# Kernel tuning notes

Measured on AMD Instinct MI355X. Metric: run time of the kernel, lower is better.

The kernel has to match this reference:

```python
import jax, jax.numpy as jnp
import numpy as np

N = 50000   # nodes
E = 400000  # edges per relation
R = 3       # relations
IN, HID, C, H = 128, 64, 40, 3  # in_feat, hidden_feat, n_classes, num_heads
NEG_SLOPE = 0.2  # DGL GATConv default leaky_relu slope


def setup_inputs() -> dict:
    key = jax.random.key(0)
    ks = jax.random.split(key, 12)
    feat = jax.random.normal(ks[0], (N, IN), jnp.float32)
    src = jax.random.randint(ks[1], (R, E), 0, N, dtype=jnp.int32)
    dst = jax.random.randint(ks[2], (R, E), 0, N, dtype=jnp.int32)

    def w(k, shape, fan):
        return jax.random.normal(k, shape, jnp.float32) / np.float32(np.sqrt(fan))

    # layer 1: in_feat -> hidden_feat, relu activation
    W1 = w(ks[3], (R, IN, H * HID), IN)
    al1 = w(ks[4], (R, H, HID), HID)
    ar1 = w(ks[5], (R, H, HID), HID)
    b1 = jnp.zeros((R, H * HID), jnp.float32)
    # layer 2: hidden_feat -> n_classes, no activation
    W2 = w(ks[6], (R, HID, H * C), HID)
    al2 = w(ks[7], (R, H, C), C)
    ar2 = w(ks[8], (R, H, C), C)
    b2 = jnp.zeros((R, H * C), jnp.float32)
    return dict(feat=feat, src=src, dst=dst, W1=W1, al1=al1, ar1=ar1, b1=b1,
                W2=W2, al2=al2, ar2=ar2, b2=b2)


def gat_hetero_layer(feat, src, dst, W, al, ar, b, apply_relu):
    """HeteroGraphConv(mean) over R relations, each a GATConv + head-mean."""
    n = feat.shape[0]

    def one_relation(src_r, dst_r, W_r, al_r, ar_r, b_r):
        n_heads, out = al_r.shape
        z = (feat @ W_r).reshape(n, n_heads, out)          # [N,H,out]
        el = jnp.sum(z * al_r, axis=-1)                    # [N,H]
        er = jnp.sum(z * ar_r, axis=-1)                    # [N,H]
        e = jax.nn.leaky_relu(el[src_r] + er[dst_r], NEG_SLOPE)  # [E,H]
        # edge softmax over incoming edges of each dst node
        m = jax.ops.segment_max(e, dst_r, num_segments=n)  # [N,H]
        a = jnp.exp(e - m[dst_r])                          # [E,H]
        s = jax.ops.segment_sum(a, dst_r, num_segments=n)  # [N,H]
        alpha = a / s[dst_r]                               # [E,H]
        msg = alpha[:, :, None] * z[src_r]                 # [E,H,out]
        rst = jax.ops.segment_sum(msg, dst_r, num_segments=n)  # [N,H,out]
        rst = rst + b_r.reshape(n_heads, out)
        if apply_relu:
            rst = jax.nn.relu(rst)
        return rst.mean(axis=1)                            # head mean -> [N,out]

    outs = jax.vmap(one_relation)(src, dst, W, al, ar, b)  # [R,N,out]
    return outs.mean(axis=0)                               # relation mean


def reference(feat, src, dst, W1, al1, ar1, b1, W2, al2, ar2, b2):
    h = gat_hetero_layer(feat, src, dst, W1, al1, ar1, b1, True)
    h = gat_hetero_layer(h, src, dst, W2, al2, ar2, b2, False)
    return h
```

## Files before the change

kernel.cpp:

```cpp
#include <hip/hip_runtime.h>

#define R_   3
#define N_   50000
#define E_   400000
#define IN_  128
#define HID_ 64
#define C_   40
#define H_   3
#define NEG_SLOPE 0.2f
#define LOG2E 1.4426950408889634f

#define SCAN_CHUNK 1024
#define NCH  49
#define NCH2 64

#define MPAD 50048
#define NRT  3128

typedef _Float16 half_t;
typedef _Float16 f16x8 __attribute__((ext_vector_type(8)));
typedef _Float16 f16x4 __attribute__((ext_vector_type(4)));
typedef float float4v __attribute__((ext_vector_type(4)));

template <int V> struct vecT;
template <> struct vecT<4> { typedef f16x4 type; };
template <> struct vecT<8> { typedef f16x8 type; };

__global__ void zero_kernel(float* __restrict__ p, size_t n) {
    size_t i = (size_t)blockIdx.x * blockDim.x + threadIdx.x;
    if (i < n) p[i] = 0.f;
}

__global__ void cast_tiled_kernel(const float* __restrict__ feat, half_t* __restrict__ At) {
    int idx = blockIdx.x * 256 + threadIdx.x;
    const int TOT = NRT * 4 * 64;
    if (idx >= TOT) return;
    int lane = idx & 63;
    int kb = (idx >> 6) & 3;
    int rowtile = idx >> 8;
    int row = rowtile * 16 + (lane & 15);
    int k = kb * 32 + (lane >> 4) * 8;
    f16x8 h = {};
    if (row < N_) {
        const float* p = feat + (size_t)row * IN_ + k;
        float4 a = ((const float4*)p)[0];
        float4 b = ((const float4*)p)[1];
        h[0] = (half_t)a.x; h[1] = (half_t)a.y; h[2] = (half_t)a.z; h[3] = (half_t)a.w;
        h[4] = (half_t)b.x; h[5] = (half_t)b.y; h[6] = (half_t)b.z; h[7] = (half_t)b.w;
    }
    ((f16x8*)At)[idx] = h;
}

template <int K, int NY>
__global__ void bprep_kernel(const float* __restrict__ W, half_t* __restrict__ Bf, int Nc) {
    constexpr int KB = K / 32;
    int idx = blockIdx.x * 256 + threadIdx.x;
    const int TOT = R_ * NY * KB * 4 * 64;
    if (idx >= TOT) return;
    int lane = idx & 63;
    int ct = (idx >> 6) & 3;
    int t = idx >> 8;
    int kb = t % KB; t /= KB;
    int y = t % NY;  int r = t / NY;
    int col = y * 64 + ct * 16 + (lane & 15);
    int k0 = kb * 32 + (lane >> 4) * 8;
    f16x8 h = {};
    if (col < Nc) {
        #pragma unroll
        for (int j = 0; j < 8; ++j)
            h[j] = (half_t)W[((size_t)r * K + k0 + j) * Nc + col];
    }
    ((f16x8*)Bf)[idx] = h;
}

__global__ void hist_kernel(const int* __restrict__ dst, int* __restrict__ deg) {
    int idx = blockIdx.x * 256 + threadIdx.x;
    if (idx < R_ * E_) {
        int r = idx / E_;
        atomicAdd(&deg[r * N_ + dst[idx]], 1);
    }
}

__global__ void scanA_kernel(const int* __restrict__ deg, int* __restrict__ bsum) {
    int r = blockIdx.y, ch = blockIdx.x, tid = threadIdx.x;
    int base = ch * SCAN_CHUNK + tid * 4;
    int s = 0;
    for (int j = 0; j < 4; ++j) {
        int i = base + j;
        if (i < N_) s += deg[r * N_ + i];
    }
    __shared__ int red[256];
    red[tid] = s; __syncthreads();
    for (int off = 128; off; off >>= 1) {
        if (tid < off) red[tid] += red[tid + off];
        __syncthreads();
    }
    if (tid == 0) bsum[r * NCH2 + ch] = red[0];
}

__global__ void scanB_kernel(int* __restrict__ bsum) {
    int w = threadIdx.x >> 6;
    int l = threadIdx.x & 63;
    if (w < R_) {
        int v = (l < NCH) ? bsum[w * NCH2 + l] : 0;
        int s = v;
        #pragma unroll
        for (int off = 1; off < 64; off <<= 1) {
            int t = __shfl_up(s, off);
            if (l >= off) s += t;
        }
        if (l < NCH) bsum[w * NCH2 + l] = s - v;
    }
}

__global__ void scanC_kernel(const int* __restrict__ deg, const int* __restrict__ bsum,
                             int* __restrict__ rowptr, int* __restrict__ cursor) {
    int r = blockIdx.y, ch = blockIdx.x, tid = threadIdx.x;
    int base = ch * SCAN_CHUNK + tid * 4;
    int v[4]; int s = 0;
    for (int j = 0; j < 4; ++j) {
        int i = base + j;
        v[j] = (i < N_) ? deg[r * N_ + i] : 0;
        s += v[j];
    }
    __shared__ int buf[256];
    buf[tid] = s; __syncthreads();
    for (int off = 1; off < 256; off <<= 1) {
        int t2 = (tid >= off) ? buf[tid - off] : 0;
        __syncthreads();
        buf[tid] += t2;
        __syncthreads();
    }
    int excl = buf[tid] - s + bsum[r * NCH2 + ch];
    int run = excl;
    for (int j = 0; j < 4; ++j) {
        int i = base + j;
        if (i < N_) {
            rowptr[r * (N_ + 1) + i] = run;
            cursor[r * N_ + i] = run;
            run += v[j];
        }
    }
    if (ch == 0 && tid == 0) rowptr[r * (N_ + 1) + N_] = E_;
}

__global__ void fill_kernel(const int* __restrict__ src, const int* __restrict__ dst,
                            int* __restrict__ cursor, int* __restrict__ csr_src) {
    int idx = blockIdx.x * 256 + threadIdx.x;
    if (idx < R_ * E_) {
        int r = idx / E_;
        int pos = atomicAdd(&cursor[r * N_ + dst[idx]], 1);
        csr_src[(size_t)r * E_ + pos] = src[idx] * 3;
    }
}

template <int K, int NY, bool FUSE>
__global__ __launch_bounds__(256) void mfma_gemm3_kernel(
        const half_t* __restrict__ At, const half_t* __restrict__ Bf,
        half_t* __restrict__ Z, int Nc,
        const float* __restrict__ al, const float* __restrict__ ar,
        float* __restrict__ el, float* __restrict__ er) {
    constexpr int KB = K / 32;
    int r = blockIdx.z, y = blockIdx.y;
    int wave = threadIdx.x >> 6, lane = threadIdx.x & 63;
    int rowtile = blockIdx.x * 4 + wave;
    const f16x8* Ap = (const f16x8*)At + (size_t)rowtile * KB * 64 + lane;
    const f16x8* Bp = (const f16x8*)Bf + (size_t)(r * NY + y) * KB * 4 * 64 + lane;
    float4v acc[4] = {};
    #pragma unroll
    for (int kb = 0; kb < KB; ++kb) {
        f16x8 af = Ap[kb * 64];
        #pragma unroll
        for (int ct = 0; ct < 4; ++ct) {
            f16x8 bf = Bp[(kb * 4 + ct) * 64];
            acc[ct] = __builtin_amdgcn_mfma_f32_16x16x32_f16(af, bf, acc[ct], 0, 0, 0);
        }
    }
    int lrow = lane & 15, lq = lane >> 4;
    half_t* Zr = Z + (size_t)r * N_ * Nc;
    int rbase = rowtile * 16 + lq * 4;
    int col0 = y * 64;
    float elv[4] = {}, erv[4] = {};
    const float* alp;
    const float* arp;
    if constexpr (FUSE) {
        alp = al + ((size_t)r * H_ + y) * 64;
        arp = ar + ((size_t)r * H_ + y) * 64;
    }
    #pragma unroll
    for (int ct = 0; ct < 4; ++ct) {
        int col = col0 + ct * 16 + lrow;
        if (col >= Nc) continue;
        float wa = 0.f, wb = 0.f;
        if constexpr (FUSE) { wa = alp[ct * 16 + lrow]; wb = arp[ct * 16 + lrow]; }
        #pragma unroll
        for (int g = 0; g < 4; ++g) {
            int row = rbase + g;
            half_t zh = (half_t)acc[ct][g];
            if (row < N_) Zr[(size_t)row * Nc + col] = zh;
            if constexpr (FUSE) {
                float zf = (float)zh;
                elv[g] = fmaf(zf, wa, elv[g]);
                erv[g] = fmaf(zf, wb, erv[g]);
            }
        }
    }
    if constexpr (FUSE) {
        #pragma unroll
        for (int g = 0; g < 4; ++g) {
            #pragma unroll
            for (int m = 1; m < 16; m <<= 1) {
                elv[g] += __shfl_xor(elv[g], m);
                erv[g] += __shfl_xor(erv[g], m);
            }
        }
        if (lrow == 0) {
            #pragma unroll
            for (int g = 0; g < 4; ++g) {
                int row = rbase + g;
                if (row < N_) {
                    size_t o = ((size_t)r * N_ + row) * H_ + y;
                    el[o] = elv[g] * LOG2E;
                    er[o] = erv[g] * LOG2E;
                }
            }
        }
    }
}

template <int Dd>
__global__ __launch_bounds__(256) void attn2_kernel(
        const half_t* __restrict__ z, const float* __restrict__ al,
        const float* __restrict__ ar, float* __restrict__ el,
        float* __restrict__ er) {
    int t = blockIdx.x * 256 + threadIdx.x;
    if (t >= R_ * N_ * H_) return;
    int rn = t / H_, h = t - rn * H_;
    int r = rn / N_;
    const half_t* zrow = z + (size_t)rn * (3 * Dd) + h * Dd;
    const float* alp = al + (r * H_ + h) * Dd;
    const float* arp = ar + (r * H_ + h) * Dd;
    float p0 = 0.f, p1 = 0.f, q0 = 0.f, q1 = 0.f;
    #pragma unroll
    for (int c = 0; c < Dd / 8; ++c) {
        f16x8 zv = *(const f16x8*)(zrow + c * 8);
        #pragma unroll
        for (int j = 0; j < 8; j += 2) {
            float za = (float)zv[j], zb = (float)zv[j + 1];
            p0 += za * alp[c * 8 + j];
            p1 += zb * alp[c * 8 + j + 1];
            q0 += za * arp[c * 8 + j];
            q1 += zb * arp[c * 8 + j + 1];
        }
    }
    el[t] = (p0 + p1) * LOG2E;
    er[t] = (q0 + q1) * LOG2E;
}

template <int Dd, int VEC, bool RELU, typename OutT, bool TILED>
__global__ __launch_bounds__(256) void agg14_kernel(
        const int* __restrict__ rowptr, const int* __restrict__ csr_src,
        const half_t* __restrict__ z, const float* __restrict__ el,
        const float* __restrict__ er, const float* __restrict__ bias,
        OutT* __restrict__ out, float scale) {
    constexpr int ROWH = 3 * Dd;
    constexpr int LPE  = ROWH / VEC;
    constexpr int PH   = Dd / VEC;
    using fv = typename vecT<VEC>::type;
    int n = blockIdx.x * 4 + (threadIdx.x >> 6);
    int lane = threadIdx.x & 63;
    if (n >= N_) return;
    int hf = lane >> 5;
    int sub = lane & 31;
    bool act = sub < LPE;
    int hl = act ? sub / PH : 0;
    int dl = act ? sub - hl * PH : 0;
    int zoff = VEC * sub;
    int ii[R_], ee[R_];
    float ervv[R_];
    #pragma unroll
    for (int r = 0; r < R_; ++r) {
        ii[r] = rowptr[r * (N_ + 1) + n];
        ee[r] = rowptr[r * (N_ + 1) + n + 1];
        ervv[r] = er[((size_t)r * N_ + n) * H_ + hl];
    }
    fv ah[R_] = {};
    float ll[R_] = {};
    while (ii[0] < ee[0] || ii[1] < ee[1] || ii[2] < ee[2]) {
        fv zA[R_], zB[R_];
        float xA[R_], xB[R_];
        bool okA[R_], okB[R_];
        #pragma unroll
        for (int r = 0; r < R_; ++r) {
            const int* cs = csr_src + (size_t)r * E_;
            const half_t* zr = z + (size_t)r * N_ * ROWH;
            const float* elr = el + (size_t)r * N_ * H_;
            int eA = ii[r] + hf, eB = ii[r] + 2 + hf;
            okA[r] = eA < ee[r];
            okB[r] = eB < ee[r];
            int sA = cs[okA[r] ? eA : 0];
            int sB = cs[okB[r] ? eB : 0];
            xA[r] = elr[sA + hl] + ervv[r];
            xB[r] = elr[sB + hl] + ervv[r];
            zA[r] = {}; zB[r] = {};
            if (act) {
                zA[r] = *(const fv*)(zr + (size_t)sA * Dd + zoff);
                zB[r] = *(const fv*)(zr + (size_t)sB * Dd + zoff);
            }
        }
        #pragma unroll
        for (int r = 0; r < R_; ++r) {
            float xa = xA[r]; xa = fmaxf(xa, NEG_SLOPE * xa);
            float xb = xB[r]; xb = fmaxf(xb, NEG_SLOPE * xb);
            float cA = okA[r] ? __builtin_amdgcn_exp2f(xa) : 0.f;
            float cB = okB[r] ? __builtin_amdgcn_exp2f(xb) : 0.f;
            ll[r] += cA + cB;
            half_t hA = (half_t)cA, hB = (half_t)cB;
            fv vA, vB;
            #pragma unroll
            for (int v = 0; v < VEC; ++v) { vA[v] = hA; vB[v] = hB; }
            ah[r] += vA * zA[r] + vB * zB[r];
        }
        #pragma unroll
        for (int r = 0; r < R_; ++r) ii[r] += 4;
    }
    float aa[R_][VEC];
    #pragma unroll
    for (int r = 0; r < R_; ++r)
        #pragma unroll
        for (int v = 0; v < VEC; ++v) aa[r][v] = (float)ah[r][v];
    #pragma unroll
    for (int r = 0; r < R_; ++r) {
        #pragma unroll
        for (int v = 0; v < VEC; ++v) aa[r][v] += __shfl(aa[r][v], lane ^ 32);
        ll[r] += __shfl(ll[r], lane ^ 32);
    }
    float vacc[VEC] = {};
    #pragma unroll
    for (int r = 0; r < R_; ++r) {
        float li = (ll[r] > 0.f) ? 1.f / ll[r] : 0.f;
        const float* br = bias + r * ROWH + hl * Dd + VEC * dl;
        #pragma unroll
        for (int v = 0; v < VEC; ++v) {
            float t = aa[r][v] * li + br[v];
            if (RELU) t = fmaxf(t, 0.f);
            vacc[v] += t;
        }
    }
    int base = lane & 32;
    int p1 = sub + PH;     if (p1 >= LPE) p1 -= LPE;
    int p2 = sub + 2 * PH; if (p2 >= LPE) p2 -= LPE;
    #pragma unroll
    for (int v = 0; v < VEC; ++v)
        vacc[v] += __shfl(vacc[v], base + p1) + __shfl(vacc[v], base + p2);
    int srcl = lane / VEC;
    int cm = lane & (VEC - 1);
    float tv[VEC];
    #pragma unroll
    for (int v = 0; v < VEC; ++v) tv[v] = __shfl(vacc[v], srcl);
    float outv = tv[0];
    #pragma unroll
    for (int v = 1; v < VEC; ++v) outv = (cm == v) ? tv[v] : outv;
    if constexpr (TILED) {
        int rowtile = n >> 4;
        int kb = lane >> 5;
        int fl = (n & 15) + ((lane >> 3) & 3) * 16;
        int elo = lane & 7;
        size_t ho = (((size_t)rowtile * 2 + kb) * 64 + fl) * 8 + elo;
        ((half_t*)out)[ho] = (half_t)(outv * scale);
    } else {
        if (lane < Dd) out[(size_t)n * Dd + lane] = (OutT)(outv * scale);
    }
}

static inline size_t align256(size_t x) { return (x + 255) & ~(size_t)255; }

extern "C" void kernel_launch(void* const* d_in, const int* in_sizes, int n_in,
                              void* d_out, int out_size, void* d_ws, size_t ws_size,
                              hipStream_t stream) {
    const float* feat = (const float*)d_in[0];
    const int*   src  = (const int*)d_in[1];
    const int*   dst  = (const int*)d_in[2];
    const float* W1   = (const float*)d_in[3];
    const float* al1  = (const float*)d_in[4];
    const float* ar1  = (const float*)d_in[5];
    const float* b1   = (const float*)d_in[6];
    const float* W2   = (const float*)d_in[7];
    const float* al2  = (const float*)d_in[8];
    const float* ar2  = (const float*)d_in[9];
    const float* b2   = (const float*)d_in[10];
    float* out = (float*)d_out;

    char* ws = (char*)d_ws;
    size_t off = 0;
    half_t* zbuf  = (half_t*)(ws + off); off += align256((size_t)R_ * N_ * (3 * HID_) * 2);
    half_t* featT = (half_t*)(ws + off); off += align256((size_t)NRT * 4 * 64 * 8 * 2);
    half_t* h1T   = (half_t*)(ws + off); off += align256((size_t)NRT * 2 * 64 * 8 * 2);
    half_t* B1f   = (half_t*)(ws + off); off += align256((size_t)R_ * 3 * 4 * 4 * 64 * 8 * 2);
    half_t* B2f   = (half_t*)(ws + off); off += align256((size_t)R_ * 2 * 2 * 4 * 64 * 8 * 2);
    float* el   = (float*)(ws + off); off += align256((size_t)R_ * N_ * H_ * 4);
    float* er   = (float*)(ws + off); off += align256((size_t)R_ * N_ * H_ * 4);
    int* deg    = (int*)(ws + off);   off += align256((size_t)R_ * N_ * 4);
    int* rowptr = (int*)(ws + off);   off += align256((size_t)R_ * (N_ + 1) * 4);
    int* cursor = (int*)(ws + off);   off += align256((size_t)R_ * N_ * 4);
    int* bsum   = (int*)(ws + off);   off += align256((size_t)R_ * NCH2 * 4);
    int* csr    = (int*)(ws + off);   off += align256((size_t)R_ * E_ * 4);
    (void)ws_size; (void)n_in; (void)in_sizes; (void)out_size;

    const int EDGE_BLOCKS = (R_ * E_ + 255) / 256;
    const int ROW_TILES = (N_ + 63) / 64;
    const int NODE_BLOCKS = (R_ * N_ + 255) / 256;
    const int NODE_WAVES = (N_ + 3) / 4;
    const int ATTN_BLOCKS = (R_ * N_ * H_ + 255) / 256;

    cast_tiled_kernel<<<(NRT * 4 * 64 + 255) / 256, 256, 0, stream>>>(feat, featT);
    bprep_kernel<IN_, 3><<<(R_ * 3 * 4 * 4 * 64 + 255) / 256, 256, 0, stream>>>(W1, B1f, H_ * HID_);
    bprep_kernel<HID_, 2><<<(R_ * 2 * 2 * 4 * 64 + 255) / 256, 256, 0, stream>>>(W2, B2f, H_ * C_);
    zero_kernel<<<7, 256, 0, stream>>>((float*)(h1T + (size_t)3125 * 2 * 512), 1536);

    zero_kernel<<<NODE_BLOCKS, 256, 0, stream>>>((float*)deg, (size_t)R_ * N_);
    hist_kernel<<<EDGE_BLOCKS, 256, 0, stream>>>(dst, deg);
    scanA_kernel<<<dim3(NCH, R_), 256, 0, stream>>>(deg, bsum);
    scanB_kernel<<<1, 192, 0, stream>>>(bsum);
    scanC_kernel<<<dim3(NCH, R_), 256, 0, stream>>>(deg, bsum, rowptr, cursor);
    fill_kernel<<<EDGE_BLOCKS, 256, 0, stream>>>(src, dst, cursor, csr);

    mfma_gemm3_kernel<IN_, 3, true><<<dim3(ROW_TILES, 3, R_), 256, 0, stream>>>(
        featT, B1f, zbuf, H_ * HID_, al1, ar1, el, er);
    agg14_kernel<HID_, 8, true, half_t, true><<<NODE_WAVES, 256, 0, stream>>>(
        rowptr, csr, zbuf, el, er, b1, h1T, 1.f / (H_ * R_));

    mfma_gemm3_kernel<HID_, 2, false><<<dim3(ROW_TILES, 2, R_), 256, 0, stream>>>(
        h1T, B2f, zbuf, H_ * C_, nullptr, nullptr, nullptr, nullptr);
    attn2_kernel<C_><<<ATTN_BLOCKS, 256, 0, stream>>>(zbuf, al2, ar2, el, er);
    agg14_kernel<C_, 4, false, float, false><<<NODE_WAVES, 256, 0, stream>>>(
        rowptr, csr, zbuf, el, er, b2, out, 1.f / (H_ * R_));
}
```

Measured before the change: 449.9 us.

## Merge prep kernels, fold scan pass, batch atomics, software-pipeline aggregation gathers

```diff
diff --git a/kernel.cpp b/kernel.cpp
--- a/kernel.cpp
+++ b/kernel.cpp
@@ -26,35 +26,11 @@
 template <> struct vecT<4> { typedef f16x4 type; };
 template <> struct vecT<8> { typedef f16x8 type; };
 
-__global__ void zero_kernel(float* __restrict__ p, size_t n) {
-    size_t i = (size_t)blockIdx.x * blockDim.x + threadIdx.x;
-    if (i < n) p[i] = 0.f;
-}
-
-__global__ void cast_tiled_kernel(const float* __restrict__ feat, half_t* __restrict__ At) {
-    int idx = blockIdx.x * 256 + threadIdx.x;
-    const int TOT = NRT * 4 * 64;
-    if (idx >= TOT) return;
-    int lane = idx & 63;
-    int kb = (idx >> 6) & 3;
-    int rowtile = idx >> 8;
-    int row = rowtile * 16 + (lane & 15);
-    int k = kb * 32 + (lane >> 4) * 8;
-    f16x8 h = {};
-    if (row < N_) {
-        const float* p = feat + (size_t)row * IN_ + k;
-        float4 a = ((const float4*)p)[0];
-        float4 b = ((const float4*)p)[1];
-        h[0] = (half_t)a.x; h[1] = (half_t)a.y; h[2] = (half_t)a.z; h[3] = (half_t)a.w;
-        h[4] = (half_t)b.x; h[5] = (half_t)b.y; h[6] = (half_t)b.z; h[7] = (half_t)b.w;
-    }
-    ((f16x8*)At)[idx] = h;
-}
 
 template <int K, int NY>
-__global__ void bprep_kernel(const float* __restrict__ W, half_t* __restrict__ Bf, int Nc) {
+__device__ inline void bprep_body(int idx, const float* __restrict__ W,
+                                  half_t* __restrict__ Bf, int Nc) {
     constexpr int KB = K / 32;
-    int idx = blockIdx.x * 256 + threadIdx.x;
     const int TOT = R_ * NY * KB * 4 * 64;
     if (idx >= TOT) return;
     int lane = idx & 63;
@@ -73,9 +49,47 @@
     ((f16x8*)Bf)[idx] = h;
 }
 
+__global__ void prep_kernel(const float* __restrict__ feat, half_t* __restrict__ At,
+                            const float* __restrict__ W1, half_t* __restrict__ B1f,
+                            const float* __restrict__ W2, half_t* __restrict__ B2f,
+                            int* __restrict__ deg, half_t* __restrict__ h1T) {
+    int b = blockIdx.x;
+    if (b < 3128) {
+        int idx = b * 256 + threadIdx.x;
+        int lane = idx & 63;
+        int kb = (idx >> 6) & 3;
+        int rowtile = idx >> 8;
+        int row = rowtile * 16 + (lane & 15);
+        int k = kb * 32 + (lane >> 4) * 8;
+        f16x8 h = {};
+        if (row < N_) {
+            const float* p = feat + (size_t)row * IN_ + k;
+            float4 a = ((const float4*)p)[0];
+            float4 c = ((const float4*)p)[1];
+            h[0] = (half_t)a.x; h[1] = (half_t)a.y; h[2] = (half_t)a.z; h[3] = (half_t)a.w;
+            h[4] = (half_t)c.x; h[5] = (half_t)c.y; h[6] = (half_t)c.z; h[7] = (half_t)c.w;
+        }
+        ((f16x8*)At)[idx] = h;
+    } else if (b < 3164) {
+        bprep_body<IN_, 3>((b - 3128) * 256 + threadIdx.x, W1, B1f, H_ * HID_);
+    } else if (b < 3188) {
+        bprep_body<HID_, 2>((b - 3164) * 256 + threadIdx.x, W2, B2f, H_ * C_);
+    } else if (b < 3774) {
+        int i = (b - 3188) * 256 + threadIdx.x;
+        if (i < R_ * N_) deg[i] = 0;
+    } else {
+        int i = (b - 3774) * 256 + threadIdx.x;
+        if (i < 3072) h1T[(size_t)3125 * 2 * 512 + i] = (half_t)0.f;
+    }
+}
+
 __global__ void hist_kernel(const int* __restrict__ dst, int* __restrict__ deg) {
-    int idx = blockIdx.x * 256 + threadIdx.x;
-    if (idx < R_ * E_) {
+    const int T = (R_ * E_) / 4;
+    int t = blockIdx.x * 256 + threadIdx.x;
+    if (t >= T) return;
+    #pragma unroll
+    for (int j = 0; j < 4; ++j) {
+        int idx = t + j * T;
         int r = idx / E_;
         atomicAdd(&deg[r * N_ + dst[idx]], 1);
     }
@@ -98,24 +112,20 @@
     if (tid == 0) bsum[r * NCH2 + ch] = red[0];
 }
 
-__global__ void scanB_kernel(int* __restrict__ bsum) {
-    int w = threadIdx.x >> 6;
-    int l = threadIdx.x & 63;
-    if (w < R_) {
-        int v = (l < NCH) ? bsum[w * NCH2 + l] : 0;
-        int s = v;
-        #pragma unroll
-        for (int off = 1; off < 64; off <<= 1) {
-            int t = __shfl_up(s, off);
-            if (l >= off) s += t;
-        }
-        if (l < NCH) bsum[w * NCH2 + l] = s - v;
-    }
-}
-
 __global__ void scanC_kernel(const int* __restrict__ deg, const int* __restrict__ bsum,
                              int* __restrict__ rowptr, int* __restrict__ cursor) {
     int r = blockIdx.y, ch = blockIdx.x, tid = threadIdx.x;
+    __shared__ int chbase_s;
+    if (tid < 64) {
+        int v = (tid < NCH) ? bsum[r * NCH2 + tid] : 0;
+        int s = v;
+        #pragma unroll
+        for (int off = 1; off < 64; off <<= 1) {
+            int t = __shfl_up(s, off);
+            if (tid >= off) s += t;
+        }
+        if (tid == ch) chbase_s = s - v;
+    }
     int base = ch * SCAN_CHUNK + tid * 4;
     int v[4]; int s = 0;
     for (int j = 0; j < 4; ++j) {
@@ -131,7 +141,7 @@
         buf[tid] += t2;
         __syncthreads();
     }
-    int excl = buf[tid] - s + bsum[r * NCH2 + ch];
+    int excl = buf[tid] - s + chbase_s;
     int run = excl;
     for (int j = 0; j < 4; ++j) {
         int i = base + j;
@@ -146,12 +156,20 @@
 
 __global__ void fill_kernel(const int* __restrict__ src, const int* __restrict__ dst,
                             int* __restrict__ cursor, int* __restrict__ csr_src) {
-    int idx = blockIdx.x * 256 + threadIdx.x;
-    if (idx < R_ * E_) {
-        int r = idx / E_;
-        int pos = atomicAdd(&cursor[r * N_ + dst[idx]], 1);
-        csr_src[(size_t)r * E_ + pos] = src[idx] * 3;
-    }
+    const int T = (R_ * E_) / 4;
+    int t = blockIdx.x * 256 + threadIdx.x;
+    if (t >= T) return;
+    int pos[4], s3[4], rr[4];
+    #pragma unroll
+    for (int j = 0; j < 4; ++j) {
+        int idx = t + j * T;
+        rr[j] = idx / E_;
+        pos[j] = atomicAdd(&cursor[rr[j] * N_ + dst[idx]], 1);
+        s3[j] = src[idx] * 3;
+    }
+    #pragma unroll
+    for (int j = 0; j < 4; ++j)
+        csr_src[(size_t)rr[j] * E_ + pos[j]] = s3[j];
 }
 
 template <int K, int NY, bool FUSE>
@@ -258,7 +276,7 @@
 }
 
 template <int Dd, int VEC, bool RELU, typename OutT, bool TILED>
-__global__ __launch_bounds__(256) void agg14_kernel(
+__global__ __launch_bounds__(256) void agg15_kernel(
         const int* __restrict__ rowptr, const int* __restrict__ csr_src,
         const half_t* __restrict__ z, const float* __restrict__ el,
         const float* __restrict__ er, const float* __restrict__ bias,
@@ -286,43 +304,86 @@
     }
     fv ah[R_] = {};
     float ll[R_] = {};
-    while (ii[0] < ee[0] || ii[1] < ee[1] || ii[2] < ee[2]) {
-        fv zA[R_], zB[R_];
-        float xA[R_], xB[R_];
-        bool okA[R_], okB[R_];
+    bool any = (ii[0] < ee[0]) | (ii[1] < ee[1]) | (ii[2] < ee[2]);
+    if (any) {
+        int sA_c[R_], sB_c[R_], sA_n[R_], sB_n[R_];
+        fv zA_c[R_], zB_c[R_];
+        float eA_c[R_], eB_c[R_];
         #pragma unroll
         for (int r = 0; r < R_; ++r) {
             const int* cs = csr_src + (size_t)r * E_;
+            int eA = ii[r] + hf, eB = ii[r] + 2 + hf;
+            sA_c[r] = cs[eA < ee[r] ? eA : 0];
+            sB_c[r] = cs[eB < ee[r] ? eB : 0];
+        }
+        #pragma unroll
+        for (int r = 0; r < R_; ++r) {
             const half_t* zr = z + (size_t)r * N_ * ROWH;
             const float* elr = el + (size_t)r * N_ * H_;
-            int eA = ii[r] + hf, eB = ii[r] + 2 + hf;
-            okA[r] = eA < ee[r];
-            okB[r] = eB < ee[r];
-            int sA = cs[okA[r] ? eA : 0];
-            int sB = cs[okB[r] ? eB : 0];
-            xA[r] = elr[sA + hl] + ervv[r];
-            xB[r] = elr[sB + hl] + ervv[r];
-            zA[r] = {}; zB[r] = {};
+            eA_c[r] = elr[sA_c[r] + hl];
+            eB_c[r] = elr[sB_c[r] + hl];
+            zA_c[r] = {}; zB_c[r] = {};
             if (act) {
-                zA[r] = *(const fv*)(zr + (size_t)sA * Dd + zoff);
-                zB[r] = *(const fv*)(zr + (size_t)sB * Dd + zoff);
+                zA_c[r] = *(const fv*)(zr + (size_t)sA_c[r] * Dd + zoff);
+                zB_c[r] = *(const fv*)(zr + (size_t)sB_c[r] * Dd + zoff);
             }
         }
         #pragma unroll
         for (int r = 0; r < R_; ++r) {
-            float xa = xA[r]; xa = fmaxf(xa, NEG_SLOPE * xa);
-            float xb = xB[r]; xb = fmaxf(xb, NEG_SLOPE * xb);
-            float cA = okA[r] ? __builtin_amdgcn_exp2f(xa) : 0.f;
-            float cB = okB[r] ? __builtin_amdgcn_exp2f(xb) : 0.f;
-            ll[r] += cA + cB;
-            half_t hA = (half_t)cA, hB = (half_t)cB;
-            fv vA, vB;
-            #pragma unroll
-            for (int v = 0; v < VEC; ++v) { vA[v] = hA; vB[v] = hB; }
-            ah[r] += vA * zA[r] + vB * zB[r];
-        }
-        #pragma unroll
-        for (int r = 0; r < R_; ++r) ii[r] += 4;
+            const int* cs = csr_src + (size_t)r * E_;
+            int eA = ii[r] + 4 + hf, eB = ii[r] + 6 + hf;
+            sA_n[r] = cs[eA < ee[r] ? eA : 0];
+            sB_n[r] = cs[eB < ee[r] ? eB : 0];
+        }
+        while (true) {
+            fv zA_n[R_], zB_n[R_];
+            float eA_n[R_], eB_n[R_];
+            #pragma unroll
+            for (int r = 0; r < R_; ++r) {
+                const half_t* zr = z + (size_t)r * N_ * ROWH;
+                const float* elr = el + (size_t)r * N_ * H_;
+                eA_n[r] = elr[sA_n[r] + hl];
+                eB_n[r] = elr[sB_n[r] + hl];
+                zA_n[r] = {}; zB_n[r] = {};
+                if (act) {
+                    zA_n[r] = *(const fv*)(zr + (size_t)sA_n[r] * Dd + zoff);
+                    zB_n[r] = *(const fv*)(zr + (size_t)sB_n[r] * Dd + zoff);
+                }
+            }
+            int sA_2[R_], sB_2[R_];
+            #pragma unroll
+            for (int r = 0; r < R_; ++r) {
+                const int* cs = csr_src + (size_t)r * E_;
+                int eA = ii[r] + 8 + hf, eB = ii[r] + 10 + hf;
+                sA_2[r] = cs[eA < ee[r] ? eA : 0];
+                sB_2[r] = cs[eB < ee[r] ? eB : 0];
+            }
+            #pragma unroll
+            for (int r = 0; r < R_; ++r) {
+                int eA = ii[r] + hf, eB = ii[r] + 2 + hf;
+                bool okA = eA < ee[r], okB = eB < ee[r];
+                float xa = eA_c[r] + ervv[r]; xa = fmaxf(xa, NEG_SLOPE * xa);
+                float xb = eB_c[r] + ervv[r]; xb = fmaxf(xb, NEG_SLOPE * xb);
+                float cA = okA ? __builtin_amdgcn_exp2f(xa) : 0.f;
+                float cB = okB ? __builtin_amdgcn_exp2f(xb) : 0.f;
+                ll[r] += cA + cB;
+                half_t hA = (half_t)cA, hB = (half_t)cB;
+                fv vA, vB;
+                #pragma unroll
+                for (int v = 0; v < VEC; ++v) { vA[v] = hA; vB[v] = hB; }
+                ah[r] += vA * zA_c[r] + vB * zB_c[r];
+            }
+            #pragma unroll
+            for (int r = 0; r < R_; ++r) ii[r] += 4;
+            if (!((ii[0] < ee[0]) | (ii[1] < ee[1]) | (ii[2] < ee[2]))) break;
+            #pragma unroll
+            for (int r = 0; r < R_; ++r) {
+                sA_c[r] = sA_n[r]; sB_c[r] = sB_n[r];
+                sA_n[r] = sA_2[r]; sB_n[r] = sB_2[r];
+                zA_c[r] = zA_n[r]; zB_c[r] = zB_n[r];
+                eA_c[r] = eA_n[r]; eB_c[r] = eB_n[r];
+            }
+        }
     }
     float aa[R_][VEC];
     #pragma unroll
@@ -407,32 +468,26 @@
     int* csr    = (int*)(ws + off);   off += align256((size_t)R_ * E_ * 4);
     (void)ws_size; (void)n_in; (void)in_sizes; (void)out_size;
 
-    const int EDGE_BLOCKS = (R_ * E_ + 255) / 256;
     const int ROW_TILES = (N_ + 63) / 64;
-    const int NODE_BLOCKS = (R_ * N_ + 255) / 256;
     const int NODE_WAVES = (N_ + 3) / 4;
     const int ATTN_BLOCKS = (R_ * N_ * H_ + 255) / 256;
-
-    cast_tiled_kernel<<<(NRT * 4 * 64 + 255) / 256, 256, 0, stream>>>(feat, featT);
-    bprep_kernel<IN_, 3><<<(R_ * 3 * 4 * 4 * 64 + 255) / 256, 256, 0, stream>>>(W1, B1f, H_ * HID_);
-    bprep_kernel<HID_, 2><<<(R_ * 2 * 2 * 4 * 64 + 255) / 256, 256, 0, stream>>>(W2, B2f, H_ * C_);
-    zero_kernel<<<7, 256, 0, stream>>>((float*)(h1T + (size_t)3125 * 2 * 512), 1536);
-
-    zero_kernel<<<NODE_BLOCKS, 256, 0, stream>>>((float*)deg, (size_t)R_ * N_);
-    hist_kernel<<<EDGE_BLOCKS, 256, 0, stream>>>(dst, deg);
+    const int E4_BLOCKS = (R_ * E_ / 4 + 255) / 256;
+
+    prep_kernel<<<3786, 256, 0, stream>>>(feat, featT, W1, B1f, W2, B2f, deg, h1T);
+
+    hist_kernel<<<E4_BLOCKS, 256, 0, stream>>>(dst, deg);
     scanA_kernel<<<dim3(NCH, R_), 256, 0, stream>>>(deg, bsum);
-    scanB_kernel<<<1, 192, 0, stream>>>(bsum);
     scanC_kernel<<<dim3(NCH, R_), 256, 0, stream>>>(deg, bsum, rowptr, cursor);
-    fill_kernel<<<EDGE_BLOCKS, 256, 0, stream>>>(src, dst, cursor, csr);
+    fill_kernel<<<E4_BLOCKS, 256, 0, stream>>>(src, dst, cursor, csr);
 
     mfma_gemm3_kernel<IN_, 3, true><<<dim3(ROW_TILES, 3, R_), 256, 0, stream>>>(
         featT, B1f, zbuf, H_ * HID_, al1, ar1, el, er);
-    agg14_kernel<HID_, 8, true, half_t, true><<<NODE_WAVES, 256, 0, stream>>>(
+    agg15_kernel<HID_, 8, true, half_t, true><<<NODE_WAVES, 256, 0, stream>>>(
         rowptr, csr, zbuf, el, er, b1, h1T, 1.f / (H_ * R_));
 
     mfma_gemm3_kernel<HID_, 2, false><<<dim3(ROW_TILES, 2, R_), 256, 0, stream>>>(
         h1T, B2f, zbuf, H_ * C_, nullptr, nullptr, nullptr, nullptr);
     attn2_kernel<C_><<<ATTN_BLOCKS, 256, 0, stream>>>(zbuf, al2, ar2, el, er);
-    agg14_kernel<C_, 4, false, float, false><<<NODE_WAVES, 256, 0, stream>>>(
+    agg15_kernel<C_, 4, false, float, false><<<NODE_WAVES, 256, 0, stream>>>(
         rowptr, csr, zbuf, el, er, b2, out, 1.f / (H_ * R_));
 }
```

After: 463.8 us. 1.03x slower.
